# Optimization experiments

Hardware: AMD Instinct MI355X
Metric: run time of the kernel (lower is better)

The kernel has to match this reference:

```python
import jax, jax.numpy as jnp
import numpy as np

B, N, D = 8, 1024, 768
H, Z = 12, 64          # num_heads, head_dim (D = H*Z)
HID = 3072             # int(D * mlp_ratio)


def setup_inputs() -> dict:
    key = jax.random.key(0)
    k1, k2, k3, k4 = jax.random.split(key, 4)
    s = 0.02
    x = jax.random.normal(k1, (B, N, D), dtype=jnp.float32)
    Wq = jax.random.normal(k2, (D, D), dtype=jnp.float32) * s
    Wk = jax.random.normal(k3, (D, D), dtype=jnp.float32) * s
    betas = jnp.full((H,), Z ** -0.5, dtype=jnp.float32)
    W_mlp = jax.random.normal(k4, (HID, D), dtype=jnp.float32) * s
    return {"x": x, "Wq": Wq, "Wk": Wk, "betas": betas, "W_mlp": W_mlp}


def reference(x, Wq, Wk, betas, W_mlp):
    # --- KQ-aligned attention ---
    # torch Linear: y = x @ W.T ; weight shape [out=D, in=D]
    Q = jnp.einsum('bnd,ed->bne', x, Wq).reshape(B, N, H, Z).transpose(0, 2, 1, 3)  # bhqz
    K = jnp.einsum('bnd,ed->bne', x, Wk).reshape(B, N, H, Z).transpose(0, 2, 1, 3)  # bhkz
    Wq_r = Wq.reshape(H, Z, D)
    Wk_r = Wk.reshape(H, Z, D)
    F1 = jnp.einsum('hzd,bhkz->bkhd', Wq_r, K)
    F2 = jnp.einsum('hzd,bhqz->bqhd', Wk_r, Q)
    scores = jnp.einsum('bhqz,bhkz,h->bhqk', Q, K, betas)
    attn = jax.nn.softmax(scores, axis=-1)
    T1 = jnp.einsum('bkhd,bhqk->bqd', F1, attn)
    T2 = jnp.einsum('bqhd,bhqk->bkd', F2, attn)
    # --- symmetric-weight Hopfield MLP (bias=False) ---
    hid = jax.nn.relu(jnp.einsum('bnd,hd->bnh', x, W_mlp))
    mlp = jnp.einsum('bnh,hd->bnd', hid, W_mlp)
    return T1 + T2 + mlp
```

## Files before the change

kernel.cpp:

```cpp
#include <hip/hip_runtime.h>
#include <hip/hip_bf16.h>

#define Bq 8
#define Nq 1024
#define Dq 768
#define Hq 12
#define Zq 64
#define HIDq 3072
#define BN (Bq*Nq)
#define QKP 1536

typedef unsigned short u16;
typedef short s16x8 __attribute__((ext_vector_type(8)));
typedef float f32x4 __attribute__((ext_vector_type(4)));
typedef unsigned short u16x4 __attribute__((ext_vector_type(4)));

#define MFMA16 __builtin_amdgcn_mfma_f32_16x16x32_bf16
#define GLOAD16(g, l) __builtin_amdgcn_global_load_lds( \
    (const __attribute__((address_space(1))) void*)(const void*)(g), \
    (__attribute__((address_space(3))) void*)(l), 16, 0, 0)

__device__ __forceinline__ u16 f2bf(float f) {
  unsigned u = __float_as_uint(f);
  return (u16)((u + 0x7FFFu + ((u >> 16) & 1u)) >> 16);
}

__device__ __forceinline__ unsigned pk2bf(float a, float b) {
  union { __hip_bfloat162 h; unsigned u; } cv;
  cv.h.x = __float2bfloat16(a);
  cv.h.y = __float2bfloat16(b);
  return cv.u;
}

__device__ __forceinline__ void xcd_swizzle(int gx, int gy, int& bx, int& by) {
  int l = blockIdx.y * gx + blockIdx.x;
  int c = l & 7, j = l >> 3;
  by = c * (gy >> 3) + j / gx;
  bx = j % gx;
}

__global__ __launch_bounds__(256) void cvt2(const float* __restrict__ x, u16* __restrict__ xb,
                                            const float* __restrict__ Wm, u16* __restrict__ Wmb) {
  int bid = blockIdx.x;
  const float* in; u16* out; int i;
  if (bid < 6144) { in = x;  out = xb;  i = bid * 1024 + threadIdx.x * 4; }
  else            { in = Wm; out = Wmb; i = (bid - 6144) * 1024 + threadIdx.x * 4; }
  float4 v = *(const float4*)&in[i];
  u16x4 o; o[0] = f2bf(v.x); o[1] = f2bf(v.y); o[2] = f2bf(v.z); o[3] = f2bf(v.w);
  *(u16x4*)&out[i] = o;
}

__global__ __launch_bounds__(256) void cvt_tr2(const float* __restrict__ Wq,
                                               const float* __restrict__ Wk,
                                               u16* __restrict__ Wqkb,
                                               u16* __restrict__ WqkT) {
  __shared__ u16 T[64][72];
  const int t = threadIdx.x;
  const int z = blockIdx.z;
  const float* in = z ? Wk : Wq;
  u16* out = Wqkb + (size_t)z * Dq * Dq;
  u16* outT = WqkT + z * Dq;
  const int r0 = blockIdx.y * 64, c0 = blockIdx.x * 64;
  const int r = t >> 3, c8 = (t & 7) * 8;
#pragma unroll
  for (int p = 0; p < 2; p++) {
    const float* ip = &in[(size_t)(r0 + r + p * 32) * Dq + c0 + c8];
    float4 v0 = *(const float4*)ip, v1 = *(const float4*)(ip + 4);
    u16 tmp[8] = {f2bf(v0.x), f2bf(v0.y), f2bf(v0.z), f2bf(v0.w),
                  f2bf(v1.x), f2bf(v1.y), f2bf(v1.z), f2bf(v1.w)};
    *(uint4*)&out[(size_t)(r0 + r + p * 32) * Dq + c0 + c8] = *(uint4*)tmp;
    *(uint4*)&T[r + p * 32][c8] = *(uint4*)tmp;
  }
  __syncthreads();
#pragma unroll
  for (int p = 0; p < 2; p++) {
    int oc = r + p * 32;
    u16 tmp[8];
#pragma unroll
    for (int j = 0; j < 8; j++) tmp[j] = T[c8 + j][oc];
    *(uint4*)&outT[(size_t)(c0 + oc) * QKP + r0 + c8] = *(uint4*)tmp;
  }
}

__global__ __launch_bounds__(256) void transpose_bf16(
    const u16* __restrict__ in, u16* __restrict__ out,
    int in_pitch, int out_pitch, int inner_n,
    long in_bs_o, long in_bs_i, long out_bs_o, long out_bs_i) {
  __shared__ u16 T[64][72];
  const int t = threadIdx.x;
  const int bz = blockIdx.z;
  const long iboff = (long)(bz / inner_n) * in_bs_o + (long)(bz % inner_n) * in_bs_i;
  const long oboff = (long)(bz / inner_n) * out_bs_o + (long)(bz % inner_n) * out_bs_i;
  const u16* ip = in + iboff + (long)(blockIdx.y * 64) * in_pitch + blockIdx.x * 64;
  u16* op = out + oboff + (long)(blockIdx.x * 64) * out_pitch + blockIdx.y * 64;
  const int r = t >> 3, c8 = (t & 7) * 8;
#pragma unroll
  for (int p = 0; p < 2; p++)
    *(uint4*)&T[r + p * 32][c8] = *(const uint4*)(ip + (size_t)(r + p * 32) * in_pitch + c8);
  __syncthreads();
#pragma unroll
  for (int p = 0; p < 2; p++) {
    int oc = r + p * 32;
    u16 tmp[8];
#pragma unroll
    for (int j = 0; j < 8; j++) tmp[j] = T[c8 + j][oc];
    *(uint4*)(op + (size_t)oc * out_pitch + c8) = *(uint4*)tmp;
  }
}

template<bool RELU, bool TRW>
__global__ __launch_bounds__(256) void gemm_bf16(
    const u16* __restrict__ A, const u16* __restrict__ B, u16* __restrict__ C,
    u16* __restrict__ QbT, u16* __restrict__ KbT,
    int M, int N, int K) {
  __shared__ u16 As[2][128 * 32];
  __shared__ u16 Bs[2][128 * 32];
  extern __shared__ u16 Ts[];
  int bx, by;
  xcd_swizzle(gridDim.x, gridDim.y, bx, by);
  const int t = threadIdx.x, l = t & 63, w = t >> 6;
  const int lq = l & 15, quad = l >> 4;
  const int bm = by * 128, bn = bx * 128;
  const int wm = (w & 1) * 64, wn = (w >> 1) * 64;
  f32x4 acc[4][4];
#pragma unroll
  for (int i = 0; i < 4; i++)
#pragma unroll
    for (int j = 0; j < 4; j++) acc[i][j] = (f32x4){0.f, 0.f, 0.f, 0.f};

  auto stage = [&](int k0, int bufi) {
#pragma unroll
    for (int p = 0; p < 2; p++) {
      int idx = p * 256 + t;
      GLOAD16(A + (size_t)(bm + (idx >> 2)) * K + k0 + (idx & 3) * 8, &As[bufi][idx * 8]);
      GLOAD16(B + (size_t)(bn + (idx >> 2)) * K + k0 + (idx & 3) * 8, &Bs[bufi][idx * 8]);
    }
  };
  stage(0, 0);
  const int nIter = K >> 5;
  for (int it = 0; it < nIter; it++) {
    __syncthreads();
    if (it + 1 < nIter) stage((it + 1) * 32, (it + 1) & 1);
    const int bi = it & 1;
    s16x8 af[4], bf[4];
#pragma unroll
    for (int mt = 0; mt < 4; mt++)
      af[mt] = *(const s16x8*)&As[bi][(wm + mt * 16 + lq) * 32 + quad * 8];
#pragma unroll
    for (int nt = 0; nt < 4; nt++)
      bf[nt] = *(const s16x8*)&Bs[bi][(wn + nt * 16 + lq) * 32 + quad * 8];
#pragma unroll
    for (int mt = 0; mt < 4; mt++)
#pragma unroll
      for (int nt = 0; nt < 4; nt++)
        acc[mt][nt] = MFMA16(af[mt], bf[nt], acc[mt][nt], 0, 0, 0);
  }
#pragma unroll
  for (int mt = 0; mt < 4; mt++)
#pragma unroll
    for (int nt = 0; nt < 4; nt++) {
      int row = bm + wm + mt * 16 + quad * 4;
      int col = bn + wn + nt * 16 + lq;
#pragma unroll
      for (int r = 0; r < 4; r++) {
        float v = acc[mt][nt][r];
        if (RELU) v = fmaxf(v, 0.f);
        C[(size_t)(row + r) * N + col] = f2bf(v);
      }
    }
  if constexpr (TRW) {
    const int b = bm >> 10, n0 = bm & 1023;
#pragma unroll
    for (int hf = 0; hf < 2; hf++) {
      __syncthreads();
      if ((w >> 1) == hf) {
#pragma unroll
        for (int mt = 0; mt < 4; mt++)
#pragma unroll
          for (int nt = 0; nt < 4; nt++)
#pragma unroll
            for (int r = 0; r < 4; r++)
              Ts[(wm + mt * 16 + quad * 4 + r) * 68 + nt * 16 + lq] =
                  f2bf(acc[mt][nt][r]);
      }
      __syncthreads();
      const int sb = bn + hf * 64;
      const int half = sb >= Dq;
      const int h = (sb - half * Dq) >> 6;
      u16* dst = (half ? KbT : QbT) + (size_t)(b * Hq + h) * 64 * Nq;
#pragma unroll
      for (int p = 0; p < 4; p++) {
        int u = p * 256 + t, zc = u >> 4, un8 = (u & 15) * 8;
        u16 tmp[8];
#pragma unroll
        for (int j = 0; j < 8; j++) tmp[j] = Ts[(un8 + j) * 68 + zc];
        *(uint4*)&dst[(size_t)zc * Nq + n0 + un8] = *(uint4*)tmp;
      }
    }
  }
}

__global__ __launch_bounds__(256) void gemm_out2(
    const u16* __restrict__ AV12, const u16* __restrict__ hid,
    const u16* __restrict__ WqkT, const u16* __restrict__ WmT,
    float* __restrict__ out) {
  __shared__ u16 As[2][128 * 64];
  __shared__ u16 Bs[2][64 * 64];
  int bx, by;
  xcd_swizzle(gridDim.x, gridDim.y, bx, by);
  const int t = threadIdx.x, l = t & 63, w = t >> 6;
  const int lq = l & 15, quad = l >> 4;
  const int bm = by * 128, bn = bx * 64;
  const int wm = w * 32;
  f32x4 acc[2][4];
#pragma unroll
  for (int i = 0; i < 2; i++)
#pragma unroll
    for (int j = 0; j < 4; j++) acc[i][j] = (f32x4){0.f, 0.f, 0.f, 0.f};

  auto stage = [&](int tl, int bufi) {
    const u16* A; const u16* B; int pitch, k0;
    if (tl < 24) { A = AV12; B = WqkT; pitch = QKP;  k0 = tl * 64; }
    else         { A = hid;  B = WmT;  pitch = HIDq; k0 = (tl - 24) * 64; }
#pragma unroll
    for (int p = 0; p < 4; p++) {
      int idx = p * 256 + t, ks = idx >> 9, rem = idx & 511;
      GLOAD16(A + (size_t)(bm + (rem >> 2)) * pitch + k0 + ks * 32 + (rem & 3) * 8,
              &As[bufi][idx * 8]);
    }
#pragma unroll
    for (int p = 0; p < 2; p++) {
      int idx = p * 256 + t, ks = idx >> 8, rem = idx & 255;
      GLOAD16(B + (size_t)(bn + (rem >> 2)) * pitch + k0 + ks * 32 + (rem & 3) * 8,
              &Bs[bufi][idx * 8]);
    }
  };
  stage(0, 0);
  for (int tl = 0; tl < 72; tl++) {
    __syncthreads();
    if (tl + 1 < 72) stage(tl + 1, (tl + 1) & 1);
    const int bi = tl & 1;
#pragma unroll
    for (int ks = 0; ks < 2; ks++) {
      s16x8 af[2], bf[4];
#pragma unroll
      for (int mt = 0; mt < 2; mt++)
        af[mt] = *(const s16x8*)&As[bi][ks * 4096 + (wm + mt * 16 + lq) * 32 + quad * 8];
#pragma unroll
      for (int nt = 0; nt < 4; nt++)
        bf[nt] = *(const s16x8*)&Bs[bi][ks * 2048 + (nt * 16 + lq) * 32 + quad * 8];
#pragma unroll
      for (int mt = 0; mt < 2; mt++)
#pragma unroll
        for (int nt = 0; nt < 4; nt++)
          acc[mt][nt] = MFMA16(af[mt], bf[nt], acc[mt][nt], 0, 0, 0);
    }
  }
#pragma unroll
  for (int mt = 0; mt < 2; mt++)
#pragma unroll
    for (int nt = 0; nt < 4; nt++) {
      int row = bm + wm + mt * 16 + quad * 4;
      int col = bn + nt * 16 + lq;
#pragma unroll
      for (int r = 0; r < 4; r++)
        out[(size_t)(row + r) * Dq + col] = acc[mt][nt][r];
    }
}

__global__ __launch_bounds__(256) void attn_pass1(
    const u16* __restrict__ QKb, const u16* __restrict__ KbT,
    const float* __restrict__ betas, u16* __restrict__ AV12,
    float* __restrict__ lg) {
  __shared__ u16 Ps[64][72];
  __shared__ u16 Ks[2][64][32];
  __shared__ u16 Kts[2][2][64][32];

  const int t = threadIdx.x, l = t & 63, w = t >> 6;
  const int lq = l & 15, quad = l >> 4;
  const int c = blockIdx.x & 7, j = blockIdx.x >> 3;
  const int bh = c * 12 + j / 16, qt = j % 16;
  const int b = bh / Hq, h = bh % Hq;
  const int q0 = qt * 64;
  const float beta = betas[h];
  const u16* Qh = QKb + (size_t)(b * Nq) * QKP + h * 64;
  const u16* Kh = Qh + Dq;
  const u16* KTh = KbT + (size_t)bh * 64 * Nq;
  u16* QsF = &Ps[0][0];
  u16* KsF = &Ks[0][0][0];

  auto stageK = [&](int kt2) {
#pragma unroll
    for (int p = 0; p < 2; p++) {
      int idx = p * 256 + t;
      GLOAD16(Kh + (size_t)(kt2 * 64 + ((idx >> 2) & 63)) * QKP + (idx >> 8) * 32 + (idx & 3) * 8,
              KsF + idx * 8);
    }
  };
  auto stageKt = [&](int kt2, int bufi) {
#pragma unroll
    for (int p = 0; p < 2; p++) {
      int idx = p * 256 + t;
      GLOAD16(KTh + (size_t)((idx >> 2) & 63) * Nq + kt2 * 64 + (idx >> 8) * 32 + (idx & 3) * 8,
              &Kts[bufi][0][0][0] + idx * 8);
    }
  };

#pragma unroll
  for (int p = 0; p < 2; p++) {
    int idx = p * 256 + t;
    GLOAD16(Qh + (size_t)(q0 + ((idx >> 2) & 63)) * QKP + (idx >> 8) * 32 + (idx & 3) * 8,
            QsF + idx * 8);
  }
  stageK(0);
  stageKt(0, 0);
  __syncthreads();
  s16x8 bqf[2][4];
#pragma unroll
  for (int zs = 0; zs < 2; zs++)
#pragma unroll
    for (int nt = 0; nt < 4; nt++)
      bqf[zs][nt] = *(const s16x8*)&QsF[zs * 2048 + (nt * 16 + lq) * 32 + quad * 8];
  __syncthreads();

  float lsum[4] = {0.f, 0.f, 0.f, 0.f};
  f32x4 ao[4];
#pragma unroll
  for (int nt = 0; nt < 4; nt++) ao[nt] = (f32x4){0.f, 0.f, 0.f, 0.f};

  for (int kt = 0; kt < 16; kt++) {
    if (kt) __syncthreads();
    const int bi = kt & 1;
    f32x4 sc[4];
#pragma unroll
    for (int nt = 0; nt < 4; nt++) sc[nt] = (f32x4){0.f, 0.f, 0.f, 0.f};
    __builtin_amdgcn_s_setprio(1);
#pragma unroll
    for (int zs = 0; zs < 2; zs++) {
      s16x8 a = *(const s16x8*)&Ks[zs][w * 16 + lq][quad * 8];
#pragma unroll
      for (int nt = 0; nt < 4; nt++)
        sc[nt] = MFMA16(a, bqf[zs][nt], sc[nt], 0, 0, 0);
    }
    __builtin_amdgcn_s_setprio(0);
#pragma unroll
    for (int nt = 0; nt < 4; nt++) {
      float e0 = __expf(sc[nt][0] * beta), e1 = __expf(sc[nt][1] * beta);
      float e2 = __expf(sc[nt][2] * beta), e3 = __expf(sc[nt][3] * beta);
      lsum[nt] += (e0 + e1) + (e2 + e3);
      uint2 pk; pk.x = pk2bf(e0, e1); pk.y = pk2bf(e2, e3);
      *(uint2*)&Ps[nt * 16 + lq][w * 16 + quad * 4] = pk;
    }
    __syncthreads();
    if (kt + 1 < 16) {
      stageK(kt + 1);
      stageKt(kt + 1, (kt + 1) & 1);
    }
    __builtin_amdgcn_s_setprio(1);
#pragma unroll
    for (int ks = 0; ks < 2; ks++) {
      s16x8 a = *(const s16x8*)&Ps[w * 16 + lq][ks * 32 + quad * 8];
#pragma unroll
      for (int nt = 0; nt < 4; nt++) {
        s16x8 bk = *(const s16x8*)&Kts[bi][ks][nt * 16 + lq][quad * 8];
        ao[nt] = MFMA16(a, bk, ao[nt], 0, 0, 0);
      }
    }
    __builtin_amdgcn_s_setprio(0);
  }
  __syncthreads();
  float* redp = (float*)&Kts[0][0][0][0];
  float* lip  = redp + 256;
#pragma unroll
  for (int nt = 0; nt < 4; nt++) {
    float v = lsum[nt];
    v += __shfl_xor(v, 16, 64);
    v += __shfl_xor(v, 32, 64);
    if (l < 16) redp[w * 64 + nt * 16 + lq] = v;
  }
  __syncthreads();
  if (t < 64) {
    float s = redp[t] + redp[64 + t] + redp[128 + t] + redp[192 + t];
    lg[(size_t)bh * Nq + q0 + t] = s;
    lip[t] = 1.0f / s;
  }
  __syncthreads();
  u16* Oh = AV12 + (size_t)(b * Nq + q0) * QKP + h * 64;
  float lr[4];
#pragma unroll
  for (int r = 0; r < 4; r++) lr[r] = lip[w * 16 + quad * 4 + r];
#pragma unroll
  for (int nt = 0; nt < 4; nt++)
#pragma unroll
    for (int r = 0; r < 4; r++)
      Oh[(size_t)(w * 16 + quad * 4 + r) * QKP + nt * 16 + lq] = f2bf(ao[nt][r] * lr[r]);
}

__global__ __launch_bounds__(256) void attn_pass2(
    const u16* __restrict__ QKb, const u16* __restrict__ QbT,
    const float* __restrict__ betas, u16* __restrict__ AV12,
    const float* __restrict__ lg) {
  __shared__ u16 Pts[64][72];
  __shared__ u16 Qs[2][64][32];
  __shared__ u16 Qts[2][2][64][32];
  __shared__ float li_s[2][64];

  const int t = threadIdx.x, l = t & 63, w = t >> 6;
  const int lq = l & 15, quad = l >> 4;
  const int c = blockIdx.x & 7, j = blockIdx.x >> 3;
  const int bh = c * 12 + j / 16, kt = j % 16;
  const int b = bh / Hq, h = bh % Hq;
  const int k0 = kt * 64;
  const float beta = betas[h];
  const u16* Qh = QKb + (size_t)(b * Nq) * QKP + h * 64;
  const u16* Kh = Qh + Dq;
  const u16* QTh = QbT + (size_t)bh * 64 * Nq;
  u16* KsF = &Pts[0][0];
  u16* QsF = &Qs[0][0][0];

  auto stageQ = [&](int qt2) {
#pragma unroll
    for (int p = 0; p < 2; p++) {
      int idx = p * 256 + t;
      GLOAD16(Qh + (size_t)(qt2 * 64 + ((idx >> 2) & 63)) * QKP + (idx >> 8) * 32 + (idx & 3) * 8,
              QsF + idx * 8);
    }
  };
  auto stageQt = [&](int qt2, int bufi) {
#pragma unroll
    for (int p = 0; p < 2; p++) {
      int idx = p * 256 + t;
      GLOAD16(QTh + (size_t)((idx >> 2) & 63) * Nq + qt2 * 64 + (idx >> 8) * 32 + (idx & 3) * 8,
              &Qts[bufi][0][0][0] + idx * 8);
    }
  };

#pragma unroll
  for (int p = 0; p < 2; p++) {
    int idx = p * 256 + t;
    GLOAD16(Kh + (size_t)(k0 + ((idx >> 2) & 63)) * QKP + (idx >> 8) * 32 + (idx & 3) * 8,
            KsF + idx * 8);
  }
  stageQ(0);
  stageQt(0, 0);
  if (t < 64) li_s[0][t] = 1.0f / lg[(size_t)bh * Nq + t];
  __syncthreads();
  s16x8 bkf[2][4];
#pragma unroll
  for (int zs = 0; zs < 2; zs++)
#pragma unroll
    for (int nt = 0; nt < 4; nt++)
      bkf[zs][nt] = *(const s16x8*)&KsF[zs * 2048 + (nt * 16 + lq) * 32 + quad * 8];
  __syncthreads();

  f32x4 ao[4];
#pragma unroll
  for (int nt = 0; nt < 4; nt++) ao[nt] = (f32x4){0.f, 0.f, 0.f, 0.f};

  for (int qt = 0; qt < 16; qt++) {
    if (qt) __syncthreads();
    const int bi = qt & 1;
    f32x4 sc[4];
#pragma unroll
    for (int nt = 0; nt < 4; nt++) sc[nt] = (f32x4){0.f, 0.f, 0.f, 0.f};
    __builtin_amdgcn_s_setprio(1);
#pragma unroll
    for (int zs = 0; zs < 2; zs++) {
      s16x8 a = *(const s16x8*)&Qs[zs][w * 16 + lq][quad * 8];
#pragma unroll
      for (int nt = 0; nt < 4; nt++)
        sc[nt] = MFMA16(a, bkf[zs][nt], sc[nt], 0, 0, 0);
    }
    __builtin_amdgcn_s_setprio(0);
    float lr[4];
#pragma unroll
    for (int r = 0; r < 4; r++) lr[r] = li_s[bi][w * 16 + quad * 4 + r];
#pragma unroll
    for (int nt = 0; nt < 4; nt++) {
      float e0 = __expf(sc[nt][0] * beta) * lr[0];
      float e1 = __expf(sc[nt][1] * beta) * lr[1];
      float e2 = __expf(sc[nt][2] * beta) * lr[2];
      float e3 = __expf(sc[nt][3] * beta) * lr[3];
      uint2 pk; pk.x = pk2bf(e0, e1); pk.y = pk2bf(e2, e3);
      *(uint2*)&Pts[nt * 16 + lq][w * 16 + quad * 4] = pk;
    }
    __syncthreads();
    if (qt + 1 < 16) {
      stageQ(qt + 1);
      stageQt(qt + 1, (qt + 1) & 1);
      if (t < 64) li_s[(qt + 1) & 1][t] = 1.0f / lg[(size_t)bh * Nq + (qt + 1) * 64 + t];
    }
    __builtin_amdgcn_s_setprio(1);
#pragma unroll
    for (int qs = 0; qs < 2; qs++) {
      s16x8 a = *(const s16x8*)&Pts[w * 16 + lq][qs * 32 + quad * 8];
#pragma unroll
      for (int nt = 0; nt < 4; nt++) {
        s16x8 bq = *(const s16x8*)&Qts[bi][qs][nt * 16 + lq][quad * 8];
        ao[nt] = MFMA16(a, bq, ao[nt], 0, 0, 0);
      }
    }
    __builtin_amdgcn_s_setprio(0);
  }
  u16* Oh = AV12 + (size_t)(b * Nq + k0) * QKP + Dq + h * 64;
#pragma unroll
  for (int nt = 0; nt < 4; nt++)
#pragma unroll
    for (int r = 0; r < 4; r++)
      Oh[(size_t)(w * 16 + quad * 4 + r) * QKP + nt * 16 + lq] = f2bf(ao[nt][r]);
}

extern "C" void kernel_launch(void* const* d_in, const int* in_sizes, int n_in,
                              void* d_out, int out_size, void* d_ws, size_t ws_size,
                              hipStream_t stream) {
  const float* x     = (const float*)d_in[0];
  const float* Wq    = (const float*)d_in[1];
  const float* Wk    = (const float*)d_in[2];
  const float* betas = (const float*)d_in[3];
  const float* Wm    = (const float*)d_in[4];
  float* out = (float*)d_out;

  u16* xb   = (u16*)d_ws;
  u16* Wqkb = xb + (size_t)BN * Dq;
  u16* Wmb  = Wqkb + (size_t)QKP * Dq;
  u16* WqkT = Wmb + (size_t)HIDq * Dq;
  u16* QKb  = WqkT + (size_t)Dq * QKP;
  u16* QbT  = QKb + (size_t)BN * QKP;
  u16* KbT  = QbT + (size_t)Bq * Hq * Zq * Nq;
  u16* AV12 = KbT + (size_t)Bq * Hq * Zq * Nq;
  float* lg = (float*)(AV12 + (size_t)BN * QKP);
  u16* hidb = QKb;
  u16* WmT  = xb;

  dim3 blk(256);
  cvt2<<<8448, blk, 0, stream>>>(x, xb, Wm, Wmb);
  cvt_tr2<<<dim3(12, 12, 2), blk, 0, stream>>>(Wq, Wk, Wqkb, WqkT);

  gemm_bf16<false, true><<<dim3(QKP / 128, BN / 128), blk, 128 * 68 * 2, stream>>>(
      xb, Wqkb, QKb, QbT, KbT, BN, QKP, Dq);

  attn_pass1<<<Bq * Hq * 16, blk, 0, stream>>>(QKb, KbT, betas, AV12, lg);
  attn_pass2<<<Bq * Hq * 16, blk, 0, stream>>>(QKb, QbT, betas, AV12, lg);

  gemm_bf16<true, false><<<dim3(HIDq / 128, BN / 128), blk, 0, stream>>>(
      xb, Wmb, hidb, nullptr, nullptr, BN, HIDq, Dq);

  transpose_bf16<<<dim3(12, 48, 1), blk, 0, stream>>>(Wmb, WmT, Dq, HIDq, 1, 0, 0, 0, 0);

  gemm_out2<<<dim3(Dq / 64, BN / 128), blk, 0, stream>>>(AV12, hidb, WqkT, WmT, out);
}
```

Before: 347.4 us.

## Software-pipeline attention passes: overlap score tile with previous PV tile

Both attention kernels are restructured so that the score/exp phase for tile k runs in the same iteration as the P·V MFMA phase for tile k-1. The K/Q and P tiles are double-buffered so each loop iteration needs one barrier instead of two, and next-tile loads are issued earlier. This is meant to cut barrier stalls and let exp/ALU work overlap with MFMA work. In exchange, shared memory per block grows, which may lower occupancy.

Result: slower. 356.5 us (+2.6%).

```diff
diff --git a/kernel.cpp b/kernel.cpp
--- a/kernel.cpp
+++ b/kernel.cpp
@@ -272,9 +272,9 @@
     const u16* __restrict__ QKb, const u16* __restrict__ KbT,
     const float* __restrict__ betas, u16* __restrict__ AV12,
     float* __restrict__ lg) {
-  __shared__ u16 Ps[64][72];
-  __shared__ u16 Ks[2][64][32];
+  __shared__ u16 Ks[2][2][64][32];
   __shared__ u16 Kts[2][2][64][32];
+  __shared__ u16 Ps[2][64][72];
 
   const int t = threadIdx.x, l = t & 63, w = t >> 6;
   const int lq = l & 15, quad = l >> 4;
@@ -286,15 +286,14 @@
   const u16* Qh = QKb + (size_t)(b * Nq) * QKP + h * 64;
   const u16* Kh = Qh + Dq;
   const u16* KTh = KbT + (size_t)bh * 64 * Nq;
-  u16* QsF = &Ps[0][0];
-  u16* KsF = &Ks[0][0][0];
-
-  auto stageK = [&](int kt2) {
+  u16* QsF = &Ps[0][0][0];
+
+  auto stageK = [&](int kt2, int bufi) {
 #pragma unroll
     for (int p = 0; p < 2; p++) {
       int idx = p * 256 + t;
       GLOAD16(Kh + (size_t)(kt2 * 64 + ((idx >> 2) & 63)) * QKP + (idx >> 8) * 32 + (idx & 3) * 8,
-              KsF + idx * 8);
+              &Ks[bufi][0][0][0] + idx * 8);
     }
   };
   auto stageKt = [&](int kt2, int bufi) {
@@ -312,8 +311,7 @@
     GLOAD16(Qh + (size_t)(q0 + ((idx >> 2) & 63)) * QKP + (idx >> 8) * 32 + (idx & 3) * 8,
             QsF + idx * 8);
   }
-  stageK(0);
-  stageKt(0, 0);
+  stageK(0, 0);
   __syncthreads();
   s16x8 bqf[2][4];
 #pragma unroll
@@ -322,22 +320,22 @@
     for (int nt = 0; nt < 4; nt++)
       bqf[zs][nt] = *(const s16x8*)&QsF[zs * 2048 + (nt * 16 + lq) * 32 + quad * 8];
   __syncthreads();
+  stageKt(0, 0);
+  stageK(1, 1);
 
   float lsum[4] = {0.f, 0.f, 0.f, 0.f};
   f32x4 ao[4];
 #pragma unroll
   for (int nt = 0; nt < 4; nt++) ao[nt] = (f32x4){0.f, 0.f, 0.f, 0.f};
 
-  for (int kt = 0; kt < 16; kt++) {
-    if (kt) __syncthreads();
-    const int bi = kt & 1;
+  auto Sphase = [&](int bi) {
     f32x4 sc[4];
 #pragma unroll
     for (int nt = 0; nt < 4; nt++) sc[nt] = (f32x4){0.f, 0.f, 0.f, 0.f};
     __builtin_amdgcn_s_setprio(1);
 #pragma unroll
     for (int zs = 0; zs < 2; zs++) {
-      s16x8 a = *(const s16x8*)&Ks[zs][w * 16 + lq][quad * 8];
+      s16x8 a = *(const s16x8*)&Ks[bi][zs][w * 16 + lq][quad * 8];
 #pragma unroll
       for (int nt = 0; nt < 4; nt++)
         sc[nt] = MFMA16(a, bqf[zs][nt], sc[nt], 0, 0, 0);
@@ -349,17 +347,14 @@
       float e2 = __expf(sc[nt][2] * beta), e3 = __expf(sc[nt][3] * beta);
       lsum[nt] += (e0 + e1) + (e2 + e3);
       uint2 pk; pk.x = pk2bf(e0, e1); pk.y = pk2bf(e2, e3);
-      *(uint2*)&Ps[nt * 16 + lq][w * 16 + quad * 4] = pk;
-    }
-    __syncthreads();
-    if (kt + 1 < 16) {
-      stageK(kt + 1);
-      stageKt(kt + 1, (kt + 1) & 1);
-    }
+      *(uint2*)&Ps[bi][nt * 16 + lq][w * 16 + quad * 4] = pk;
+    }
+  };
+  auto PVphase = [&](int bi) {
     __builtin_amdgcn_s_setprio(1);
 #pragma unroll
     for (int ks = 0; ks < 2; ks++) {
-      s16x8 a = *(const s16x8*)&Ps[w * 16 + lq][ks * 32 + quad * 8];
+      s16x8 a = *(const s16x8*)&Ps[bi][w * 16 + lq][ks * 32 + quad * 8];
 #pragma unroll
       for (int nt = 0; nt < 4; nt++) {
         s16x8 bk = *(const s16x8*)&Kts[bi][ks][nt * 16 + lq][quad * 8];
@@ -367,8 +362,19 @@
       }
     }
     __builtin_amdgcn_s_setprio(0);
-  }
-  __syncthreads();
+  };
+
+  Sphase(0);
+  for (int kt = 1; kt < 16; kt++) {
+    __syncthreads();
+    if (kt + 1 < 16) stageK(kt + 1, (kt + 1) & 1);
+    stageKt(kt, kt & 1);
+    Sphase(kt & 1);
+    PVphase((kt - 1) & 1);
+  }
+  __syncthreads();
+  PVphase(1);
+
   float* redp = (float*)&Kts[0][0][0][0];
   float* lip  = redp + 256;
 #pragma unroll
@@ -400,9 +406,9 @@
     const u16* __restrict__ QKb, const u16* __restrict__ QbT,
     const float* __restrict__ betas, u16* __restrict__ AV12,
     const float* __restrict__ lg) {
-  __shared__ u16 Pts[64][72];
-  __shared__ u16 Qs[2][64][32];
+  __shared__ u16 Qs[2][2][64][32];
   __shared__ u16 Qts[2][2][64][32];
+  __shared__ u16 Pts[2][64][72];
   __shared__ float li_s[2][64];
 
   const int t = threadIdx.x, l = t & 63, w = t >> 6;
@@ -415,15 +421,14 @@
   const u16* Qh = QKb + (size_t)(b * Nq) * QKP + h * 64;
   const u16* Kh = Qh + Dq;
   const u16* QTh = QbT + (size_t)bh * 64 * Nq;
-  u16* KsF = &Pts[0][0];
-  u16* QsF = &Qs[0][0][0];
-
-  auto stageQ = [&](int qt2) {
+  u16* KsF = &Pts[0][0][0];
+
+  auto stageQ = [&](int qt2, int bufi) {
 #pragma unroll
     for (int p = 0; p < 2; p++) {
       int idx = p * 256 + t;
       GLOAD16(Qh + (size_t)(qt2 * 64 + ((idx >> 2) & 63)) * QKP + (idx >> 8) * 32 + (idx & 3) * 8,
-              QsF + idx * 8);
+              &Qs[bufi][0][0][0] + idx * 8);
     }
   };
   auto stageQt = [&](int qt2, int bufi) {
@@ -441,8 +446,7 @@
     GLOAD16(Kh + (size_t)(k0 + ((idx >> 2) & 63)) * QKP + (idx >> 8) * 32 + (idx & 3) * 8,
             KsF + idx * 8);
   }
-  stageQ(0);
-  stageQt(0, 0);
+  stageQ(0, 0);
   if (t < 64) li_s[0][t] = 1.0f / lg[(size_t)bh * Nq + t];
   __syncthreads();
   s16x8 bkf[2][4];
@@ -452,21 +456,22 @@
     for (int nt = 0; nt < 4; nt++)
       bkf[zs][nt] = *(const s16x8*)&KsF[zs * 2048 + (nt * 16 + lq) * 32 + quad * 8];
   __syncthreads();
+  stageQt(0, 0);
+  stageQ(1, 1);
+  if (t < 64) li_s[1][t] = 1.0f / lg[(size_t)bh * Nq + 64 + t];
 
   f32x4 ao[4];
 #pragma unroll
   for (int nt = 0; nt < 4; nt++) ao[nt] = (f32x4){0.f, 0.f, 0.f, 0.f};
 
-  for (int qt = 0; qt < 16; qt++) {
-    if (qt) __syncthreads();
-    const int bi = qt & 1;
+  auto Sphase = [&](int bi) {
     f32x4 sc[4];
 #pragma unroll
     for (int nt = 0; nt < 4; nt++) sc[nt] = (f32x4){0.f, 0.f, 0.f, 0.f};
     __builtin_amdgcn_s_setprio(1);
 #pragma unroll
     for (int zs = 0; zs < 2; zs++) {
-      s16x8 a = *(const s16x8*)&Qs[zs][w * 16 + lq][quad * 8];
+      s16x8 a = *(const s16x8*)&Qs[bi][zs][w * 16 + lq][quad * 8];
 #pragma unroll
       for (int nt = 0; nt < 4; nt++)
         sc[nt] = MFMA16(a, bkf[zs][nt], sc[nt], 0, 0, 0);
@@ -482,18 +487,14 @@
       float e2 = __expf(sc[nt][2] * beta) * lr[2];
       float e3 = __expf(sc[nt][3] * beta) * lr[3];
       uint2 pk; pk.x = pk2bf(e0, e1); pk.y = pk2bf(e2, e3);
-      *(uint2*)&Pts[nt * 16 + lq][w * 16 + quad * 4] = pk;
-    }
-    __syncthreads();
-    if (qt + 1 < 16) {
-      stageQ(qt + 1);
-      stageQt(qt + 1, (qt + 1) & 1);
-      if (t < 64) li_s[(qt + 1) & 1][t] = 1.0f / lg[(size_t)bh * Nq + (qt + 1) * 64 + t];
-    }
+      *(uint2*)&Pts[bi][nt * 16 + lq][w * 16 + quad * 4] = pk;
+    }
+  };
+  auto PVphase = [&](int bi) {
     __builtin_amdgcn_s_setprio(1);
 #pragma unroll
     for (int qs = 0; qs < 2; qs++) {
-      s16x8 a = *(const s16x8*)&Pts[w * 16 + lq][qs * 32 + quad * 8];
+      s16x8 a = *(const s16x8*)&Pts[bi][w * 16 + lq][qs * 32 + quad * 8];
 #pragma unroll
       for (int nt = 0; nt < 4; nt++) {
         s16x8 bq = *(const s16x8*)&Qts[bi][qs][nt * 16 + lq][quad * 8];
@@ -501,7 +502,23 @@
       }
     }
     __builtin_amdgcn_s_setprio(0);
-  }
+  };
+
+  Sphase(0);
+  for (int qt2 = 1; qt2 < 16; qt2++) {
+    __syncthreads();
+    if (qt2 + 1 < 16) {
+      stageQ(qt2 + 1, (qt2 + 1) & 1);
+      if (t < 64)
+        li_s[(qt2 + 1) & 1][t] = 1.0f / lg[(size_t)bh * Nq + (qt2 + 1) * 64 + t];
+    }
+    stageQt(qt2, qt2 & 1);
+    Sphase(qt2 & 1);
+    PVphase((qt2 - 1) & 1);
+  }
+  __syncthreads();
+  PVphase(1);
+
   u16* Oh = AV12 + (size_t)(b * Nq + k0) * QKP + Dq + h * 64;
 #pragma unroll
   for (int nt = 0; nt < 4; nt++)
```
